# Optimization experiments

Measured on AMD Instinct MI355X. Metric: run time of the kernel, lower is better.

The kernel has to match this reference:

```python
import jax, jax.numpy as jnp
import numpy as np

B, D_DATA, D_DICT0, N_SAE, D_DICT = 2048, 768, 128, 128, 32


def _kaiming_uniform(key, shape, fan_in):
    # torch.nn.init.kaiming_uniform_ default: bound = sqrt(6 / fan_in) / sqrt(5-gain stuff) ~ use gain=sqrt(2)? match torch default a=sqrt(5) not needed; plain kaiming_uniform_ uses gain=sqrt(2): bound = sqrt(6/fan_in)*? Keep simple: bound = sqrt(6.0/fan_in)
    bound = np.sqrt(6.0 / fan_in)
    return jax.random.uniform(key, shape, jnp.float32, -bound, bound)


def setup_inputs() -> dict:
    key = jax.random.key(0)
    ks = jax.random.split(key, 6)
    x = jax.random.normal(ks[0], (B, D_DATA), jnp.float32)
    # top-level SAE params
    W_enc0 = _kaiming_uniform(ks[1], (D_DATA, D_DICT0), D_DATA)
    b_enc0 = jnp.zeros((D_DICT0,), jnp.float32)
    W_dec0 = _kaiming_uniform(ks[2], (D_DICT0, D_DATA), D_DICT0)
    W_dec0 = W_dec0 / jnp.linalg.norm(W_dec0, axis=-1, keepdims=True)
    b_dec0 = jnp.zeros((D_DATA,), jnp.float32)
    # sublayer (hierarchical) per-expert params
    W_enc1 = _kaiming_uniform(ks[3], (N_SAE, D_DATA, D_DICT), D_DATA)
    b_enc1 = jnp.zeros((N_SAE, D_DICT), jnp.float32)
    W_dec1 = _kaiming_uniform(ks[4], (N_SAE, D_DICT, D_DATA), D_DICT)
    W_dec1 = W_dec1 / jnp.linalg.norm(W_dec1, axis=-1, keepdims=True)
    b_dec1 = jnp.zeros((N_SAE, D_DATA), jnp.float32)
    return {"x": x, "W_enc0": W_enc0, "b_enc0": b_enc0, "W_dec0": W_dec0,
            "b_dec0": b_dec0, "W_enc1": W_enc1, "b_enc1": b_enc1,
            "W_dec1": W_dec1, "b_dec1": b_dec1}


def reference(x, W_enc0, b_enc0, W_dec0, b_dec0, W_enc1, b_enc1, W_dec1, b_dec1):
    # ---- sae_0 (standard SAE; scale/unscale are identity) ----
    acts0 = jax.nn.relu((x - b_dec0) @ W_enc0 + b_enc0)        # [B, D_DICT0]
    x0 = acts0 @ W_dec0 + b_dec0                               # [B, D_DATA]
    # ---- binary gate over experts (n_sae == d_dict0) ----
    gate = (acts0 > 0).astype(x.dtype)                         # [B, N_SAE]
    # ---- sublayer: gather-encode-decode-scatter, expressed densely with a
    # binary mask (gate only selects membership; gate value is not multiplied).
    # Avoid materializing [B, N_SAE, D_DATA] by distributing (x - b_dec1[j]):
    pre = (jnp.einsum('bd,jdk->bjk', x, W_enc1)
           - jnp.einsum('jd,jdk->jk', b_dec1, W_enc1)[None]
           + b_enc1[None])                                     # [B, N_SAE, D_DICT]
    acts1 = jax.nn.relu(pre) * gate[:, :, None]                # zero out ungated
    # scatter_add over experts: sum_j gated (acts1[b,j] @ W_dec1[j] + b_dec1[j])
    dec = jnp.einsum('bjk,jkd->bd', acts1, W_dec1) + gate @ b_dec1  # [B, D_DATA]
    return x0 + dec
```

## Files before the change

### kernel.cpp

```cpp
#include <hip/hip_runtime.h>
#include <hip/hip_bf16.h>
#include <stdint.h>

#define B_SZ   2048
#define DDATA  768
#define NSAE   128
#define NJK    4096
#define KA2    4352
#define SPLITK 4
#define KC2    1088
#define B2TB   816

typedef unsigned short u16;
typedef short bf16x8 __attribute__((ext_vector_type(8)));
typedef float f32x4  __attribute__((ext_vector_type(4)));

static __device__ __forceinline__ u16 f2bf(float f) {
  __hip_bfloat16 h = __float2bfloat16(f);
  return *reinterpret_cast<u16*>(&h);
}

static __device__ __forceinline__ void gload16(const u16* g, u16* l) {
  __builtin_amdgcn_global_load_lds(
      (const __attribute__((address_space(1))) unsigned int*)g,
      (__attribute__((address_space(3))) unsigned int*)l,
      16, 0, 0);
}

__global__ __launch_bounds__(256) void k_front(const float* __restrict__ x,
                                               const float* __restrict__ We0,
                                               const float* __restrict__ be0,
                                               const float* __restrict__ bd0,
                                               const float* __restrict__ We1,
                                               const float* __restrict__ bd1,
                                               const float* __restrict__ be1,
                                               u16* __restrict__ W1T,
                                               float* __restrict__ cvp,
                                               u16* __restrict__ xb,
                                               u16* __restrict__ A2) {
  __shared__ float smem[6280];
  const int bid = blockIdx.x, t = threadIdx.x;
  if (bid < 512) {
    const int b0 = bid * 4;
    float* xs   = smem;
    float* part = smem + 3072;
    float* wqp  = smem + 5120;
    float* xns  = smem + 5632;
#pragma unroll
    for (int i = 0; i < 3; ++i) {
      int idx = t + i * 256;
      int r = idx / 192, c4 = idx % 192;
      size_t go = (size_t)(b0 + r) * DDATA + c4 * 4;
      float4 v = *(const float4*)&x[go];
      ushort4 o;
      o.x = f2bf(v.x); o.y = f2bf(v.y); o.z = f2bf(v.z); o.w = f2bf(v.w);
      *(ushort4*)&xb[go] = o;
      float4 b4 = *(const float4*)&bd0[c4 * 4];
      v.x -= b4.x; v.y -= b4.y; v.z -= b4.z; v.w -= b4.w;
      *(float4*)&xs[r * DDATA + c4 * 4] = v;
    }
    __syncthreads();
    const int ln = t & 63, w = t >> 6;
    {
      float a = 0.f;
#pragma unroll
      for (int q = 0; q < 12; ++q) { float xv = xs[w * DDATA + ln + q * 64]; a += xv * xv; }
#pragma unroll
      for (int sh = 32; sh; sh >>= 1) a += __shfl_xor(a, sh, 64);
      if (ln == 0) xns[w] = a;
    }
    const int j0 = ln * 2;
    float a00=0.f,a01=0.f,a10=0.f,a11=0.f,a20=0.f,a21=0.f,a30=0.f,a31=0.f;
    float wq0=0.f, wq1=0.f;
    const int dbase = w * 192;
    for (int d = dbase; d < dbase + 192; d += 4) {
      float4 xv0 = *(const float4*)&xs[0 * DDATA + d];
      float4 xv1 = *(const float4*)&xs[1 * DDATA + d];
      float4 xv2 = *(const float4*)&xs[2 * DDATA + d];
      float4 xv3 = *(const float4*)&xs[3 * DDATA + d];
#pragma unroll
      for (int dd = 0; dd < 4; ++dd) {
        float2 w2 = *(const float2*)&We0[(size_t)(d + dd) * 128 + j0];
        float x0 = ((const float*)&xv0)[dd], x1 = ((const float*)&xv1)[dd];
        float x2 = ((const float*)&xv2)[dd], x3 = ((const float*)&xv3)[dd];
        a00 += x0 * w2.x; a01 += x0 * w2.y;
        a10 += x1 * w2.x; a11 += x1 * w2.y;
        a20 += x2 * w2.x; a21 += x2 * w2.y;
        a30 += x3 * w2.x; a31 += x3 * w2.y;
        wq0 += w2.x * w2.x; wq1 += w2.y * w2.y;
      }
    }
    *(float2*)&part[(w * 4 + 0) * 128 + j0] = make_float2(a00, a01);
    *(float2*)&part[(w * 4 + 1) * 128 + j0] = make_float2(a10, a11);
    *(float2*)&part[(w * 4 + 2) * 128 + j0] = make_float2(a20, a21);
    *(float2*)&part[(w * 4 + 3) * 128 + j0] = make_float2(a30, a31);
    *(float2*)&wqp[w * 128 + j0] = make_float2(wq0, wq1);
    __syncthreads();
    float p0 = be0[j0], p1 = be0[j0 + 1];
    float wn0 = 0.f, wn1 = 0.f;
#pragma unroll
    for (int q = 0; q < 4; ++q) {
      float2 pr = *(const float2*)&part[(q * 4 + w) * 128 + j0];
      p0 += pr.x; p1 += pr.y;
      float2 wr2 = *(const float2*)&wqp[q * 128 + j0];
      wn0 += wr2.x; wn1 += wr2.y;
    }
    const float sx = sqrtf(xns[w]);
    const float tau0 = 1e-4f * sx * sqrtf(wn0);
    const float tau1 = 1e-4f * sx * sqrtf(wn1);
    const int bb = b0 + w;
    const size_t row = (size_t)bb * KA2;
    unsigned pk = (unsigned)f2bf(p0 > 0.f ? p0 : 0.f) |
                  ((unsigned)f2bf(p1 > 0.f ? p1 : 0.f) << 16);
    unsigned gk = (p0 > 0.f ? 0x3F80u : 0u) | (p1 > 0.f ? 0x3F800000u : 0u);
    *(unsigned*)&A2[row + NJK + j0]       = pk;
    *(unsigned*)&A2[row + NJK + 128 + j0] = gk;
#pragma unroll
    for (int c = 0; c < 2; ++c) {
      float pv = c ? p1 : p0;
      float tv = c ? tau1 : tau0;
      unsigned long long mask = __ballot(fabsf(pv) <= tv);
      while (mask) {
        int src = (int)__builtin_ctzll(mask);
        mask &= mask - 1;
        int jj = src * 2 + c;
        double acc = 0.0;
#pragma unroll
        for (int q = 0; q < 12; ++q) {
          int d = ln + q * 64;
          acc += (double)(x[(size_t)bb * DDATA + d] - bd0[d]) *
                 (double)We0[(size_t)d * 128 + jj];
        }
#pragma unroll
        for (int sh = 32; sh; sh >>= 1) acc += __shfl_xor(acc, sh, 64);
        if (ln == src) {
          double pd = acc + (double)be0[jj];
          A2[row + NJK + jj]       = f2bf(pd > 0.0 ? (float)pd : 0.f);
          A2[row + NJK + 128 + jj] = (pd > 0.0) ? (u16)0x3F80 : (u16)0;
        }
      }
    }
  } else {
    const int e = bid - 512;
    const int j = e & 127, seg = e >> 7;
    float* ts  = smem;
    float* bds = smem + 64 * 33;
    float* red = smem + 64 * 33 + 64;
    const int k = t & 31, g = t >> 5;
    float cacc = 0.f;
    for (int db = seg * 4; db < seg * 4 + 4; ++db) {
      const float* src = We1 + (size_t)j * 24576 + db * 2048;
#pragma unroll
      for (int i = 0; i < 8; ++i) {
        int ee = t + i * 256;
        ts[(ee >> 5) * 33 + (ee & 31)] = src[ee];
      }
      if (t < 64) bds[t] = bd1[(size_t)j * DDATA + db * 64 + t];
      __syncthreads();
#pragma unroll
      for (int i = 0; i < 8; ++i) {
        int ee = t + i * 256;
        int kk = ee >> 6, d = ee & 63;
        W1T[(size_t)(j * 32 + kk) * DDATA + db * 64 + d] = f2bf(ts[d * 33 + kk]);
      }
#pragma unroll
      for (int q = 0; q < 8; ++q) {
        int d = g + 8 * q;
        cacc += ts[d * 33 + k] * bds[d];
      }
      __syncthreads();
    }
    red[g * 32 + k] = cacc;
    __syncthreads();
    if (g == 0) {
      float s = 0.f;
#pragma unroll
      for (int q = 0; q < 8; ++q) s += red[q * 32 + k];
      cvp[seg * 4096 + j * 32 + k] = (seg == 0 ? be1[j * 32 + k] : 0.f) - s;
    }
  }
}

template<int BM, int BN, int EPI>
__global__ __launch_bounds__(256) void k_gemm(const u16* __restrict__ A,
                                              const u16* __restrict__ Bm,
                                              int K, int Kc,
                                              float* __restrict__ outF,
                                              u16* __restrict__ A2,
                                              const float* __restrict__ cvec,
                                              const float* __restrict__ Wd1,
                                              const float* __restrict__ Wd0,
                                              const float* __restrict__ bd1,
                                              u16* __restrict__ B2Tp) {
  constexpr int WM = BM / 32, WN = BN / 32;
  __shared__ __align__(16) u16 AsBs[(BM + BN) * 64];
  __shared__ u16 gate_s[BM * 4];
  __shared__ float cv_s[BN];
  const int tid = threadIdx.x;
  const int h = blockIdx.x;

  if (EPI == 1 && h < B2TB) {
    float* fsm = (float*)&AsBs[0];
    const int rb = h / 12, dbk = h % 12;
    const float* src; int r0, base;
    if (rb < 64)      { src = Wd1; r0 = rb * 64;        base = 0;    }
    else if (rb < 66) { src = Wd0; r0 = (rb - 64) * 64; base = 4096; }
    else              { src = bd1; r0 = (rb - 66) * 64; base = 4224; }
    const int d0 = dbk * 64;
#pragma unroll
    for (int i = 0; i < 16; ++i) {
      int ee = tid + i * 256;
      int ri = ee >> 6, di = ee & 63;
      fsm[ri * 65 + di] = src[(size_t)(r0 + ri) * DDATA + d0 + di];
    }
    __syncthreads();
#pragma unroll
    for (int i = 0; i < 16; ++i) {
      int ee = tid + i * 256;
      int di = ee >> 6, ri = ee & 63;
      B2Tp[(size_t)(d0 + di) * KA2 + base + r0 + ri] = f2bf(fsm[ri * 65 + di]);
    }
    return;
  }

  int bx, by, bz;
  if (EPI == 1) {
    const int hg = h - B2TB;
    const int l = (hg & 7) * 128 + (hg >> 3);
    const int g2 = l >> 7, w = l & 127;
    by = w >> 2; bx = (g2 << 2) + (w & 3); bz = 0;
  } else {
    const int l = (h & 7) * 96 + (h >> 3);
    bx = l >> 7; const int r2 = l & 127; bz = r2 >> 5; by = r2 & 31;
  }
  const int kbase = bz * Kc;
  const u16* Ab = A  + (size_t)(by * BM) * K;
  const u16* Bb = Bm + (size_t)(bx * BN) * K;
  const int wave = tid >> 6, lane = tid & 63;
  const int wr = wave >> 1, wc = wave & 1;
  const int m0 = wr * (BM / 2), n0 = wc * (BN / 2);
  const int lm = lane & 15, qd = lane >> 4;
  u16* As = &AsBs[0];
  u16* Bs = &AsBs[BM * 64];

  if (EPI == 1) {
    for (int e = tid; e < BM * 4; e += 256) {
      int r = e >> 2, q = e & 3;
      gate_s[e] = A2[(size_t)(by * BM + r) * KA2 + NJK + 128 + bx * 4 + q];
    }
    for (int e = tid; e < BN; e += 256)
      cv_s[e] = cvec[bx * BN + e] + cvec[4096 + bx * BN + e] + cvec[8192 + bx * BN + e];
  }

  f32x4 acc[WM][WN];
  const f32x4 zero = {0.f, 0.f, 0.f, 0.f};
  for (int mi = 0; mi < WM; ++mi)
    for (int ni = 0; ni < WN; ++ni) acc[mi][ni] = zero;

  for (int k0 = kbase; k0 < kbase + Kc; k0 += 64) {
#pragma unroll
    for (int i = 0; i < BM / 32; ++i) {
      int id = tid + 256 * i;
      int row = id >> 3, u = id & 7;
      gload16(Ab + (size_t)row * K + k0 + ((u ^ (row & 7)) * 8), &As[id * 8]);
    }
#pragma unroll
    for (int i = 0; i < BN / 32; ++i) {
      int id = tid + 256 * i;
      int row = id >> 3, u = id & 7;
      gload16(Bb + (size_t)row * K + k0 + ((u ^ (row & 7)) * 8), &Bs[id * 8]);
    }
    __syncthreads();
#pragma unroll
    for (int s = 0; s < 2; ++s) {
      const int swz = ((s << 2) + qd) ^ (lm & 7);
      bf16x8 af[WM], bfv[WN];
#pragma unroll
      for (int mi = 0; mi < WM; ++mi)
        af[mi] = *(const bf16x8*)&As[(m0 + mi * 16 + lm) * 64 + swz * 8];
#pragma unroll
      for (int ni = 0; ni < WN; ++ni)
        bfv[ni] = *(const bf16x8*)&Bs[(n0 + ni * 16 + lm) * 64 + swz * 8];
#pragma unroll
      for (int mi = 0; mi < WM; ++mi)
#pragma unroll
        for (int ni = 0; ni < WN; ++ni)
          acc[mi][ni] = __builtin_amdgcn_mfma_f32_16x16x32_bf16(af[mi], bfv[ni],
                                                                acc[mi][ni], 0, 0, 0);
    }
    __syncthreads();
  }

  const int rb = qd * 4;
#pragma unroll
  for (int mi = 0; mi < WM; ++mi) {
#pragma unroll
    for (int ni = 0; ni < WN; ++ni) {
#pragma unroll
      for (int r = 0; r < 4; ++r) {
        int ml = m0 + mi * 16 + rb + r;
        int nl = n0 + ni * 16 + lm;
        int gm = by * BM + ml;
        int gn = bx * BN + nl;
        float v = acc[mi][ni][r];
        if (EPI == 1) {
          v += cv_s[nl];
          v = v > 0.f ? v : 0.f;
          u16 gbit = gate_s[ml * 4 + (nl >> 5)];
          v = gbit ? v : 0.f;
          float vn = __shfl_xor(v, 1, 64);
          if ((lm & 1) == 0) {
            unsigned pk = (unsigned)f2bf(v) | ((unsigned)f2bf(vn) << 16);
            *(unsigned*)&A2[(size_t)gm * KA2 + gn] = pk;
          }
        } else {
          outF[((size_t)bz * B_SZ + gm) * DDATA + gn] = v;
        }
      }
    }
  }
}

__global__ __launch_bounds__(256) void k_reduce(const float* __restrict__ part,
                                                const float* __restrict__ bias,
                                                float* __restrict__ out) {
  const int N4 = B_SZ * DDATA / 4;
  int i = blockIdx.x * 256 + threadIdx.x;
  const float4* p4 = (const float4*)part;
  float4 s = p4[i];
#pragma unroll
  for (int z = 1; z < SPLITK; ++z) {
    float4 t = p4[i + z * N4];
    s.x += t.x; s.y += t.y; s.z += t.z; s.w += t.w;
  }
  float4 b = ((const float4*)bias)[i % (DDATA / 4)];
  s.x += b.x; s.y += b.y; s.z += b.z; s.w += b.w;
  ((float4*)out)[i] = s;
}

extern "C" void kernel_launch(void* const* d_in, const int* in_sizes, int n_in,
                              void* d_out, int out_size, void* d_ws, size_t ws_size,
                              hipStream_t stream) {
  const float* x   = (const float*)d_in[0];
  const float* We0 = (const float*)d_in[1];
  const float* be0 = (const float*)d_in[2];
  const float* Wd0 = (const float*)d_in[3];
  const float* bd0 = (const float*)d_in[4];
  const float* We1 = (const float*)d_in[5];
  const float* be1 = (const float*)d_in[6];
  const float* Wd1 = (const float*)d_in[7];
  const float* bd1 = (const float*)d_in[8];
  float* out = (float*)d_out;

  uint8_t* ws = (uint8_t*)d_ws;
  size_t off = 0;
  auto carve = [&](size_t bytes) {
    uint8_t* p = ws + off;
    off += (bytes + 255) & ~(size_t)255;
    return p;
  };
  u16*    A2   = (u16*)carve((size_t)B_SZ * KA2 * 2);
  u16*    xb   = (u16*)carve((size_t)B_SZ * DDATA * 2);
  u16*    W1T  = (u16*)carve((size_t)NJK * DDATA * 2);
  u16*    B2T  = (u16*)carve((size_t)DDATA * KA2 * 2);
  float*  cvp  = (float*)carve((size_t)3 * NJK * 4);
  float*  part = (float*)carve((size_t)SPLITK * B_SZ * DDATA * 4);

  k_front <<<896, 256, 0, stream>>>(x, We0, be0, bd0, We1, bd1, be1,
                                    W1T, cvp, xb, A2);
  k_gemm<64, 128, 1><<<B2TB + 1024, 256, 0, stream>>>(
      xb, W1T, DDATA, DDATA, nullptr, A2, cvp, Wd1, Wd0, bd1, B2T);
  k_gemm<64, 128, 2><<<768, 256, 0, stream>>>(
      A2, B2T, KA2, KC2, part, nullptr, nullptr, nullptr, nullptr, nullptr, nullptr);
  k_reduce<<<1536, 256, 0, stream>>>(part, bd0, out);
}
```

Before: 155.8 us.

## Use 128x128 tiles with in-kernel split-K for the expert encoder GEMM

Result: slower. 257.6 us (+65.3%).

```diff
diff --git a/kernel.cpp b/kernel.cpp
--- a/kernel.cpp
+++ b/kernel.cpp
@@ -10,6 +10,7 @@
 #define SPLITK 4
 #define KC2    1088
 #define B2TB   816
+#define G1TILES 512
 
 typedef unsigned short u16;
 typedef short bf16x8 __attribute__((ext_vector_type(8)));
@@ -37,7 +38,8 @@
                                                u16* __restrict__ W1T,
                                                float* __restrict__ cvp,
                                                u16* __restrict__ xb,
-                                               u16* __restrict__ A2) {
+                                               u16* __restrict__ A2,
+                                               unsigned* __restrict__ cnt) {
   __shared__ float smem[6280];
   const int bid = blockIdx.x, t = threadIdx.x;
   if (bid < 512) {
@@ -140,7 +142,7 @@
         }
       }
     }
-  } else {
+  } else if (bid < 896) {
     const int e = bid - 512;
     const int j = e & 127, seg = e >> 7;
     float* ts  = smem;
@@ -178,6 +180,9 @@
       for (int q = 0; q < 8; ++q) s += red[q * 32 + k];
       cvp[seg * 4096 + j * 32 + k] = (seg == 0 ? be1[j * 32 + k] : 0.f) - s;
     }
+  } else {
+    cnt[t] = 0u;
+    cnt[t + 256] = 0u;
   }
 }
 
@@ -191,11 +196,14 @@
                                               const float* __restrict__ Wd1,
                                               const float* __restrict__ Wd0,
                                               const float* __restrict__ bd1,
-                                              u16* __restrict__ B2Tp) {
+                                              u16* __restrict__ B2Tp,
+                                              float* __restrict__ partG1,
+                                              unsigned* __restrict__ cnt) {
   constexpr int WM = BM / 32, WN = BN / 32;
   __shared__ __align__(16) u16 AsBs[(BM + BN) * 64];
   __shared__ u16 gate_s[BM * 4];
   __shared__ float cv_s[BN];
+  __shared__ unsigned who_s;
   const int tid = threadIdx.x;
   const int h = blockIdx.x;
 
@@ -227,8 +235,12 @@
   if (EPI == 1) {
     const int hg = h - B2TB;
     const int l = (hg & 7) * 128 + (hg >> 3);
-    const int g2 = l >> 7, w = l & 127;
-    by = w >> 2; bx = (g2 << 2) + (w & 3); bz = 0;
+    const int g2 = l >> 7;
+    const int w = l & 127;
+    const int tl = w >> 1;
+    bz = w & 1;
+    by = tl >> 2;
+    bx = (g2 << 2) + (tl & 3);
   } else {
     const int l = (h & 7) * 96 + (h >> 3);
     bx = l >> 7; const int r2 = l & 127; bz = r2 >> 5; by = r2 & 31;
@@ -292,18 +304,40 @@
   }
 
   const int rb = qd * 4;
-#pragma unroll
-  for (int mi = 0; mi < WM; ++mi) {
-#pragma unroll
-    for (int ni = 0; ni < WN; ++ni) {
-#pragma unroll
-      for (int r = 0; r < 4; ++r) {
-        int ml = m0 + mi * 16 + rb + r;
-        int nl = n0 + ni * 16 + lm;
-        int gm = by * BM + ml;
-        int gn = bx * BN + nl;
-        float v = acc[mi][ni][r];
-        if (EPI == 1) {
+  if (EPI == 1) {
+    const int tileid = by * 32 + bx;
+    float* myp = partG1 + ((size_t)(bz * G1TILES + tileid)) * (BM * BN);
+#pragma unroll
+    for (int mi = 0; mi < WM; ++mi)
+#pragma unroll
+      for (int ni = 0; ni < WN; ++ni)
+#pragma unroll
+        for (int r = 0; r < 4; ++r) {
+          int ml = m0 + mi * 16 + rb + r;
+          int nl = n0 + ni * 16 + lm;
+          myp[ml * BN + nl] = acc[mi][ni][r];
+        }
+    __syncthreads();
+    if (tid == 0) {
+      __threadfence();
+      who_s = atomicAdd(&cnt[tileid], 1u);
+    }
+    __syncthreads();
+    if (who_s == 0) return;
+    if (tid == 0) __threadfence();
+    __syncthreads();
+    const float* op = partG1 + ((size_t)((1 - bz) * G1TILES + tileid)) * (BM * BN);
+#pragma unroll
+    for (int mi = 0; mi < WM; ++mi) {
+#pragma unroll
+      for (int ni = 0; ni < WN; ++ni) {
+#pragma unroll
+        for (int r = 0; r < 4; ++r) {
+          int ml = m0 + mi * 16 + rb + r;
+          int nl = n0 + ni * 16 + lm;
+          int gm = by * BM + ml;
+          int gn = bx * BN + nl;
+          float v = acc[mi][ni][r] + op[ml * BN + nl];
           v += cv_s[nl];
           v = v > 0.f ? v : 0.f;
           u16 gbit = gate_s[ml * 4 + (nl >> 5)];
@@ -313,11 +347,22 @@
             unsigned pk = (unsigned)f2bf(v) | ((unsigned)f2bf(vn) << 16);
             *(unsigned*)&A2[(size_t)gm * KA2 + gn] = pk;
           }
-        } else {
-          outF[((size_t)bz * B_SZ + gm) * DDATA + gn] = v;
         }
       }
     }
+  } else {
+#pragma unroll
+    for (int mi = 0; mi < WM; ++mi)
+#pragma unroll
+      for (int ni = 0; ni < WN; ++ni)
+#pragma unroll
+        for (int r = 0; r < 4; ++r) {
+          int ml = m0 + mi * 16 + rb + r;
+          int nl = n0 + ni * 16 + lm;
+          int gm = by * BM + ml;
+          int gn = bx * BN + nl;
+          outF[((size_t)bz * B_SZ + gm) * DDATA + gn] = acc[mi][ni][r];
+        }
   }
 }
 
@@ -359,18 +404,21 @@
     off += (bytes + 255) & ~(size_t)255;
     return p;
   };
-  u16*    A2   = (u16*)carve((size_t)B_SZ * KA2 * 2);
-  u16*    xb   = (u16*)carve((size_t)B_SZ * DDATA * 2);
-  u16*    W1T  = (u16*)carve((size_t)NJK * DDATA * 2);
-  u16*    B2T  = (u16*)carve((size_t)DDATA * KA2 * 2);
-  float*  cvp  = (float*)carve((size_t)3 * NJK * 4);
-  float*  part = (float*)carve((size_t)SPLITK * B_SZ * DDATA * 4);
-
-  k_front <<<896, 256, 0, stream>>>(x, We0, be0, bd0, We1, bd1, be1,
-                                    W1T, cvp, xb, A2);
-  k_gemm<64, 128, 1><<<B2TB + 1024, 256, 0, stream>>>(
-      xb, W1T, DDATA, DDATA, nullptr, A2, cvp, Wd1, Wd0, bd1, B2T);
+  u16*      A2   = (u16*)carve((size_t)B_SZ * KA2 * 2);
+  u16*      xb   = (u16*)carve((size_t)B_SZ * DDATA * 2);
+  u16*      W1T  = (u16*)carve((size_t)NJK * DDATA * 2);
+  u16*      B2T  = (u16*)carve((size_t)DDATA * KA2 * 2);
+  float*    cvp  = (float*)carve((size_t)3 * NJK * 4);
+  float*    part = (float*)carve((size_t)SPLITK * B_SZ * DDATA * 4);
+  float*    pG1  = (float*)carve((size_t)2 * G1TILES * 128 * 128 * 4);
+  unsigned* cnt  = (unsigned*)carve((size_t)G1TILES * 4);
+
+  k_front <<<897, 256, 0, stream>>>(x, We0, be0, bd0, We1, bd1, be1,
+                                    W1T, cvp, xb, A2, cnt);
+  k_gemm<128, 128, 1><<<B2TB + 1024, 256, 0, stream>>>(
+      xb, W1T, DDATA, 384, nullptr, A2, cvp, Wd1, Wd0, bd1, B2T, pG1, cnt);
   k_gemm<64, 128, 2><<<768, 256, 0, stream>>>(
-      A2, B2T, KA2, KC2, part, nullptr, nullptr, nullptr, nullptr, nullptr, nullptr);
+      A2, B2T, KA2, KC2, part, nullptr, nullptr, nullptr, nullptr, nullptr,
+      nullptr, nullptr, nullptr);
   k_reduce<<<1536, 256, 0, stream>>>(part, bd0, out);
 }
```
